# Performance work log

Hardware: AMD Instinct MI355X
Metric: run time of the kernel (lower is better)

Reference implementation:

```python
import jax, jax.numpy as jnp
import numpy as np

N_NODES = 100000
EPS = 1e-12  # F.normalize default eps


def _sage_conv(x, edge_index, Wl, bl, Wr):
    # PyG SAGEConv, aggr='mean', normalize=True.
    # edge_index[0] = source j, edge_index[1] = target i; messages flow j -> i.
    src, dst = edge_index[0], edge_index[1]
    msg_sum = jax.ops.segment_sum(x[src], dst, num_segments=N_NODES)  # [N, F]
    cnt = jax.ops.segment_sum(jnp.ones_like(src, dtype=x.dtype), dst,
                              num_segments=N_NODES)                  # [N]
    mean = msg_sum / jnp.maximum(cnt, 1.0)[:, None]  # empty neighborhoods -> 0
    out = mean @ Wl + bl + x @ Wr                    # lin_l(aggr) + lin_r(x)
    norm = jnp.sqrt(jnp.sum(out * out, axis=-1, keepdims=True))
    return out / jnp.maximum(norm, EPS)              # row-wise L2 normalize


def setup_inputs() -> dict:
    key = jax.random.key(0)
    ks = jax.random.split(key, 8)
    F_IN, F_HID, F_OUT = 64, 64, 32
    x = jax.random.normal(ks[0], (N_NODES, F_IN), dtype=jnp.float32)
    edge_index = jax.random.randint(ks[1], (2, 1000000), 0, N_NODES, dtype=jnp.int64)
    s1 = 1.0 / np.sqrt(F_IN)
    s2 = 1.0 / np.sqrt(F_HID)
    return {
        "x": x,
        "edge_index": edge_index,
        "W1l": jax.random.normal(ks[2], (F_IN, F_HID), dtype=jnp.float32) * s1,
        "b1": jnp.zeros((F_HID,), dtype=jnp.float32),
        "W1r": jax.random.normal(ks[3], (F_IN, F_HID), dtype=jnp.float32) * s1,
        "W2l": jax.random.normal(ks[4], (F_HID, F_OUT), dtype=jnp.float32) * s2,
        "b2": jnp.zeros((F_OUT,), dtype=jnp.float32),
        "W2r": jax.random.normal(ks[5], (F_HID, F_OUT), dtype=jnp.float32) * s2,
    }


def reference(x, edge_index, W1l, b1, W1r, W2l, b2, W2r):
    # eval mode: dropout(p=0.6) is identity
    h = jax.nn.relu(_sage_conv(x, edge_index, W1l, b1, W1r))
    out = _sage_conv(h, edge_index, W2l, b2, W2r)
    return out
```

## Files before the change

kernel.cpp:

```cpp
#include <hip/hip_runtime.h>

#define NN 100000
#define NE 1000000
#define NBK 391
#define CAP 3328
#define CH 8192
#define NCB ((NE + CH - 1) / CH)
#define PREP_ITEMS (NN * 16 + 64 + 64 * 128 + 32 * 128)
#define NPREPB ((PREP_ITEMS + 511) / 512)
#define XS 24.0f
#define HS 127.0f

typedef __attribute__((ext_vector_type(8))) short bf16x8;
typedef __attribute__((ext_vector_type(4))) float f32x4;

__device__ __forceinline__ ushort f2bf(float f) {
    uint u = __builtin_bit_cast(uint, f);
    u += 0x7FFFu + ((u >> 16) & 1u);
    return (ushort)(u >> 16);
}
__device__ __forceinline__ uint pack2(float a, float b) {
    uint ua = __builtin_bit_cast(uint, a), ub = __builtin_bit_cast(uint, b);
    ua += 0x7FFFu + ((ua >> 16) & 1u);
    ub += 0x7FFFu + ((ub >> 16) & 1u);
    return (ua >> 16) | (ub & 0xFFFF0000u);
}

__device__ __forceinline__ uint packi8(float4 v, float s) {
    int q0 = (int)rintf(fminf(fmaxf(v.x * s, -127.f), 127.f));
    int q1 = (int)rintf(fminf(fmaxf(v.y * s, -127.f), 127.f));
    int q2 = (int)rintf(fminf(fmaxf(v.z * s, -127.f), 127.f));
    int q3 = (int)rintf(fminf(fmaxf(v.w * s, -127.f), 127.f));
    return (q0 & 255) | ((q1 & 255) << 8) | ((q2 & 255) << 16) | ((q3 & 255) << 24);
}

#define DEC4(w, A0, A1, A2, A3)                                            \
    A0 += (float)((int)((w) << 24) >> 24);                                 \
    A1 += (float)((int)((w) << 16) >> 24);                                 \
    A2 += (float)((int)((w) << 8) >> 24);                                  \
    A3 += (float)((int)(w) >> 24);

#define ACCQ(p)                                                            \
    DEC4(p.x, a0, a1, a2, a3) DEC4(p.y, a4, a5, a6, a7)                    \
    DEC4(p.z, b0, b1, b2, b3) DEC4(p.w, b4, b5, b6, b7)


__global__ __launch_bounds__(512) void prep_bin(
    const float* __restrict__ x, uint* __restrict__ xb2, uint* __restrict__ x8w,
    const float* __restrict__ W1l, const float* __restrict__ W1r,
    const float* __restrict__ W2l, const float* __restrict__ W2r,
    ushort* __restrict__ W1t, ushort* __restrict__ W2t,
    uint* __restrict__ hb2, uint* __restrict__ h8w,
    const int* __restrict__ src, const int* __restrict__ dst,
    int* __restrict__ gcur, uint* __restrict__ binned) {
    int tid = threadIdx.x;
    if (blockIdx.x < NCB) {
        __shared__ int lh[NBK + 1], lb[NBK + 1], lr[NBK + 1];
        for (int i = tid; i < NBK + 1; i += 512) { lh[i] = 0; lr[i] = 0; }
        __syncthreads();
        int base = blockIdx.x * CH;
#pragma unroll
        for (int k = 0; k < 16; ++k) {
            int e = base + tid + k * 512;
            if (e < NE) atomicAdd(&lh[dst[e] >> 8], 1);
        }
        __syncthreads();
        if (tid < NBK && lh[tid] > 0)
            lb[tid] = tid * CAP + atomicAdd(&gcur[tid], lh[tid]);
        __syncthreads();
#pragma unroll
        for (int k = 0; k < 16; ++k) {
            int e = base + tid + k * 512;
            if (e < NE) {
                int d = dst[e];
                int bk = d >> 8;
                int r = atomicAdd(&lr[bk], 1);
                binned[lb[bk] + r] = (uint)src[e] | ((uint)(d & 255) << 24);
            }
        }
        return;
    }
    int t = (blockIdx.x - NCB) * 512 + tid;
    if (t < NN * 16) {
        float4 v = reinterpret_cast<const float4*>(x)[t];
        uint2 o;
        o.x = pack2(v.x, v.y);
        o.y = pack2(v.z, v.w);
        reinterpret_cast<uint2*>(xb2)[t] = o;
        int n = t >> 4, f0 = (t & 15) * 4;
        int pos = (f0 < 32) ? ((f0 >> 3) * 16 + (f0 & 7))
                            : (((f0 - 32) >> 3) * 16 + 8 + (f0 & 7));
        x8w[n * 16 + (pos >> 2)] = packi8(v, XS);
    } else {
        int z = t - NN * 16;
        if (z < 16) {
            uint2 o; o.x = 0u; o.y = 0u;
            reinterpret_cast<uint2*>(xb2)[NN * 16 + z] = o;
        } else if (z < 32) {
            uint2 o; o.x = 0u; o.y = 0u;
            reinterpret_cast<uint2*>(hb2)[NN * 16 + (z - 16)] = o;
        } else if (z < 48) {
            x8w[NN * 16 + (z - 32)] = 0u;
        } else if (z < 64) {
            h8w[NN * 16 + (z - 48)] = 0u;
        } else {
            int u = z - 64;
            if (u < 64 * 128) {
                int f = u >> 7, k = u & 127;
                float v = (k < 64) ? W1l[k * 64 + f] : W1r[(k - 64) * 64 + f];
                W1t[u] = f2bf(v);
            } else if (u < 64 * 128 + 32 * 128) {
                int p = u - 64 * 128;
                int f = p >> 7, k = p & 127;
                float v = (k < 64) ? W2l[k * 32 + f] : W2r[(k - 64) * 32 + f];
                W2t[p] = f2bf(v);
            }
        }
    }
}

__global__ __launch_bounds__(256) void sort_bucket(const uint* __restrict__ binned,
                                                   const int* __restrict__ gcur,
                                                   uint* __restrict__ ssrc,
                                                   uint* __restrict__ offp) {
    __shared__ uint recs[CAP];
    __shared__ int cnt[256], sc[256], cur[256];
    int b = blockIdx.x, t = threadIdx.x;
    int s = b * CAP, n = gcur[b];
    cnt[t] = 0;
    __syncthreads();
    for (int i = t; i < n; i += 256) {
        uint r = binned[s + i];
        recs[i] = r;
        atomicAdd(&cnt[r >> 24], 1);
    }
    __syncthreads();
    int c = cnt[t];
    int pc = (c + 3) & ~3;
    sc[t] = pc;
    for (int d = 1; d < 256; d <<= 1) {
        __syncthreads();
        int add = (t >= d) ? sc[t - d] : 0;
        __syncthreads();
        sc[t] += add;
    }
    __syncthreads();
    int ex = sc[t] - pc;
    cur[t] = ex;
    int node = b * 256 + t;
    if (node < NN) offp[node] = (uint)(s + ex) | ((uint)c << 22);
    __syncthreads();
    for (int i = t; i < n; i += 256) {
        uint r = recs[i];
        int p = atomicAdd(&cur[r >> 24], 1);
        ssrc[s + p] = r & 0xFFFFFFu;
    }
    for (int z = ex + c; z < ex + pc; ++z) ssrc[s + z] = NN;
}

__global__ __launch_bounds__(256) void layer1_fused(
    const uint4* __restrict__ x8v, const ushort* __restrict__ xb,
    const uint* __restrict__ offp, const uint* __restrict__ ssrc,
    const ushort* __restrict__ Wt, const float* __restrict__ bias,
    ushort* __restrict__ hb, uchar* __restrict__ h8) {
    int w = threadIdx.x >> 6, l = threadIdx.x & 63;
    int r = l & 15, q = l >> 4;
    int node0 = blockIdx.x * 64 + w * 16;
    int node = node0 + r;
    int beg = 0, c = 0;
    if (node < NN) {
        uint p = offp[node];
        beg = (int)(p & 0x3FFFFFu);
        c = (int)(p >> 22);
    }
    int rem = (c + 3) & ~3;
    float a0=0.f,a1=0.f,a2=0.f,a3=0.f,a4=0.f,a5=0.f,a6=0.f,a7=0.f;
    float b0=0.f,b1=0.f,b2=0.f,b3=0.f,b4=0.f,b5=0.f,b6=0.f,b7=0.f;
    int i = beg;
    uint j0 = 0, j1 = 0, j2 = 0, j3 = 0;
    if (rem > 0) { j0 = ssrc[i]; j1 = ssrc[i+1]; j2 = ssrc[i+2]; j3 = ssrc[i+3]; }
    while (rem > 0) {
        uint4 p0 = x8v[(size_t)j0 * 4 + q];
        uint4 p1 = x8v[(size_t)j1 * 4 + q];
        uint4 p2 = x8v[(size_t)j2 * 4 + q];
        uint4 p3 = x8v[(size_t)j3 * 4 + q];
        i += 4; rem -= 4;
        if (rem > 0) { j0 = ssrc[i]; j1 = ssrc[i+1]; j2 = ssrc[i+2]; j3 = ssrc[i+3]; }
        ACCQ(p0) ACCQ(p1) ACCQ(p2) ACCQ(p3)
    }
    float inv = 1.f / (fmaxf((float)c, 1.f) * XS);
    uint4 mu, mv;
    mu.x = pack2(a0 * inv, a1 * inv); mu.y = pack2(a2 * inv, a3 * inv);
    mu.z = pack2(a4 * inv, a5 * inv); mu.w = pack2(a6 * inv, a7 * inv);
    mv.x = pack2(b0 * inv, b1 * inv); mv.y = pack2(b2 * inv, b3 * inv);
    mv.z = pack2(b4 * inv, b5 * inv); mv.w = pack2(b6 * inv, b7 * inv);
    bf16x8 afr0 = __builtin_bit_cast(bf16x8, mu);
    bf16x8 afr1 = __builtin_bit_cast(bf16x8, mv);
    int arow = (node < NN) ? node : 0;
    const ushort* ax = xb + (size_t)arow * 64 + q * 8;
    bf16x8 afr2 = *reinterpret_cast<const bf16x8*>(ax);
    bf16x8 afr3 = *reinterpret_cast<const bf16x8*>(ax + 32);

    f32x4 c0 = {0.f, 0.f, 0.f, 0.f}, c1 = c0, c2 = c0, c3 = c0;
    const ushort* wp = Wt + (size_t)r * 128 + q * 8;
#pragma unroll
    for (int ks = 0; ks < 4; ++ks) {
        const ushort* wk = wp + ks * 32;
        bf16x8 w0 = *reinterpret_cast<const bf16x8*>(wk);
        bf16x8 w1 = *reinterpret_cast<const bf16x8*>(wk + 16 * 128);
        bf16x8 w2 = *reinterpret_cast<const bf16x8*>(wk + 32 * 128);
        bf16x8 w3 = *reinterpret_cast<const bf16x8*>(wk + 48 * 128);
        bf16x8 af = (ks == 0) ? afr0 : (ks == 1) ? afr1 : (ks == 2) ? afr2 : afr3;
        c0 = __builtin_amdgcn_mfma_f32_16x16x32_bf16(af, w0, c0, 0, 0, 0);
        c1 = __builtin_amdgcn_mfma_f32_16x16x32_bf16(af, w1, c1, 0, 0, 0);
        c2 = __builtin_amdgcn_mfma_f32_16x16x32_bf16(af, w2, c2, 0, 0, 0);
        c3 = __builtin_amdgcn_mfma_f32_16x16x32_bf16(af, w3, c3, 0, 0, 0);
    }
    float bb0 = bias[r], bb1 = bias[16 + r], bb2 = bias[32 + r], bb3 = bias[48 + r];
#pragma unroll
    for (int reg = 0; reg < 4; ++reg) {
        c0[reg] += bb0; c1[reg] += bb1; c2[reg] += bb2; c3[reg] += bb3;
    }
    int pr = (r >> 3) * 16, pj = r & 7;
#pragma unroll
    for (int reg = 0; reg < 4; ++reg) {
        float s = c0[reg] * c0[reg] + c1[reg] * c1[reg] +
                  c2[reg] * c2[reg] + c3[reg] * c3[reg];
        s += __shfl_xor(s, 1, 64);
        s += __shfl_xor(s, 2, 64);
        s += __shfl_xor(s, 4, 64);
        s += __shfl_xor(s, 8, 64);
        float scl = 1.f / fmaxf(sqrtf(s), 1e-12f);
        int grow = node0 + q * 4 + reg;
        if (grow < NN) {
            float v0 = fmaxf(c0[reg] * scl, 0.f);
            float v1 = fmaxf(c1[reg] * scl, 0.f);
            float v2 = fmaxf(c2[reg] * scl, 0.f);
            float v3 = fmaxf(c3[reg] * scl, 0.f);
            ushort* hp = hb + (size_t)grow * 64 + r;
            hp[0]  = f2bf(v0);
            hp[16] = f2bf(v1);
            hp[32] = f2bf(v2);
            hp[48] = f2bf(v3);
            uchar* hp8 = h8 + (size_t)grow * 64;
            hp8[pr + pj]           = (uchar)(int)rintf(v0 * HS);
            hp8[pr + 32 + pj]      = (uchar)(int)rintf(v1 * HS);
            hp8[pr + 8 + pj]       = (uchar)(int)rintf(v2 * HS);
            hp8[pr + 40 + pj]      = (uchar)(int)rintf(v3 * HS);
        }
    }
}

__global__ __launch_bounds__(256) void layer2_fused(
    const uint4* __restrict__ h8v, const ushort* __restrict__ hbuf,
    const uint* __restrict__ offp, const uint* __restrict__ ssrc,
    const ushort* __restrict__ Wt, const float* __restrict__ bias,
    float* __restrict__ out) {
    int w = threadIdx.x >> 6, l = threadIdx.x & 63;
    int r = l & 15, q = l >> 4;
    int node0 = blockIdx.x * 64 + w * 16;
    int node = node0 + r;
    int beg = 0, c = 0;
    if (node < NN) {
        uint p = offp[node];
        beg = (int)(p & 0x3FFFFFu);
        c = (int)(p >> 22);
    }
    int rem = (c + 3) & ~3;
    float a0=0.f,a1=0.f,a2=0.f,a3=0.f,a4=0.f,a5=0.f,a6=0.f,a7=0.f;
    float b0=0.f,b1=0.f,b2=0.f,b3=0.f,b4=0.f,b5=0.f,b6=0.f,b7=0.f;
    int i = beg;
    uint j0 = 0, j1 = 0, j2 = 0, j3 = 0;
    if (rem > 0) { j0 = ssrc[i]; j1 = ssrc[i+1]; j2 = ssrc[i+2]; j3 = ssrc[i+3]; }
    while (rem > 0) {
        uint4 p0 = h8v[(size_t)j0 * 4 + q];
        uint4 p1 = h8v[(size_t)j1 * 4 + q];
        uint4 p2 = h8v[(size_t)j2 * 4 + q];
        uint4 p3 = h8v[(size_t)j3 * 4 + q];
        i += 4; rem -= 4;
        if (rem > 0) { j0 = ssrc[i]; j1 = ssrc[i+1]; j2 = ssrc[i+2]; j3 = ssrc[i+3]; }
        ACCQ(p0) ACCQ(p1) ACCQ(p2) ACCQ(p3)
    }
    float inv = 1.f / (fmaxf((float)c, 1.f) * HS);
    uint4 mu, mv;
    mu.x = pack2(a0 * inv, a1 * inv); mu.y = pack2(a2 * inv, a3 * inv);
    mu.z = pack2(a4 * inv, a5 * inv); mu.w = pack2(a6 * inv, a7 * inv);
    mv.x = pack2(b0 * inv, b1 * inv); mv.y = pack2(b2 * inv, b3 * inv);
    mv.z = pack2(b4 * inv, b5 * inv); mv.w = pack2(b6 * inv, b7 * inv);
    bf16x8 afr0 = __builtin_bit_cast(bf16x8, mu);
    bf16x8 afr1 = __builtin_bit_cast(bf16x8, mv);
    int arow = (node < NN) ? node : 0;
    const ushort* ax = hbuf + (size_t)arow * 64 + q * 8;
    bf16x8 afr2 = *reinterpret_cast<const bf16x8*>(ax);
    bf16x8 afr3 = *reinterpret_cast<const bf16x8*>(ax + 32);

    f32x4 c0 = {0.f, 0.f, 0.f, 0.f}, c1 = c0;
    const ushort* wp = Wt + (size_t)r * 128 + q * 8;
#pragma unroll
    for (int ks = 0; ks < 4; ++ks) {
        const ushort* wk = wp + ks * 32;
        bf16x8 w0 = *reinterpret_cast<const bf16x8*>(wk);
        bf16x8 w1 = *reinterpret_cast<const bf16x8*>(wk + 16 * 128);
        bf16x8 af = (ks == 0) ? afr0 : (ks == 1) ? afr1 : (ks == 2) ? afr2 : afr3;
        c0 = __builtin_amdgcn_mfma_f32_16x16x32_bf16(af, w0, c0, 0, 0, 0);
        c1 = __builtin_amdgcn_mfma_f32_16x16x32_bf16(af, w1, c1, 0, 0, 0);
    }
    float bb0 = bias[r], bb1 = bias[16 + r];
#pragma unroll
    for (int reg = 0; reg < 4; ++reg) { c0[reg] += bb0; c1[reg] += bb1; }
#pragma unroll
    for (int reg = 0; reg < 4; ++reg) {
        float s = c0[reg] * c0[reg] + c1[reg] * c1[reg];
        s += __shfl_xor(s, 1, 64);
        s += __shfl_xor(s, 2, 64);
        s += __shfl_xor(s, 4, 64);
        s += __shfl_xor(s, 8, 64);
        float scl = 1.f / fmaxf(sqrtf(s), 1e-12f);
        int grow = node0 + q * 4 + reg;
        if (grow < NN) {
            float* op = out + (size_t)grow * 32 + r;
            op[0]  = c0[reg] * scl;
            op[16] = c1[reg] * scl;
        }
    }
}

extern "C" void kernel_launch(void* const* d_in, const int* in_sizes, int n_in,
                              void* d_out, int out_size, void* d_ws, size_t ws_size,
                              hipStream_t stream) {
    const float* x   = (const float*)d_in[0];
    const int*   ei  = (const int*)d_in[1];
    const int*   src = ei;
    const int*   dst = ei + NE;
    const float* W1l = (const float*)d_in[2];
    const float* b1  = (const float*)d_in[3];
    const float* W1r = (const float*)d_in[4];
    const float* W2l = (const float*)d_in[5];
    const float* b2  = (const float*)d_in[6];
    const float* W2r = (const float*)d_in[7];
    float* out = (float*)d_out;

    ushort* xb   = (ushort*)d_ws;
    ushort* hb   = xb + (size_t)(NN + 1) * 64;
    uchar*  x8   = (uchar*)(hb + (size_t)(NN + 1) * 64);
    uchar*  h8   = x8 + (size_t)(NN + 1) * 64;
    ushort* W1t  = (ushort*)(h8 + (size_t)(NN + 1) * 64);
    ushort* W2t  = W1t + 64 * 128;
    int*    gcur = (int*)(W2t + 32 * 128);
    uint*   offp = (uint*)(gcur + NBK + 1);
    uint*   binn = (uint*)(offp + NN);
    uint*   ssrc = binn + (size_t)NBK * CAP;

    hipMemsetAsync(gcur, 0, (NBK + 1) * sizeof(int), stream);

    prep_bin   <<<NCB + NPREPB, 512, 0, stream>>>(
                   x, (uint*)xb, (uint*)x8, W1l, W1r, W2l, W2r, W1t, W2t,
                   (uint*)hb, (uint*)h8, src, dst, gcur, binn);
    sort_bucket<<<NBK, 256, 0, stream>>>(binn, gcur, ssrc, offp);

    layer1_fused<<<(NN + 63) / 64, 256, 0, stream>>>(
                    (const uint4*)x8, xb, offp, ssrc, W1t, b1, hb, h8);
    layer2_fused<<<(NN + 63) / 64, 256, 0, stream>>>(
                    (const uint4*)h8, hb, offp, ssrc, W2t, b2, out);
}
```

Measured before the change: 97.21 us.

## Drop bf16 copy of x, use wave-shuffle scan, and widen gather unroll

The prep kernel no longer writes a bf16 copy of x. Layer 1 now reads the fp32 x rows directly and converts them to bf16 in registers, which removes a full-size write and read of that buffer. sort_bucket replaces the barrier-heavy shared-memory Hillis-Steele scan with a per-wave shuffle scan plus a combine across wave sums. Both gather loops now process 8 neighbors per iteration with the index loads issued inline rather than prefetched. In exchange, layer 1 reads twice as many bytes for its self term, and the prefetch of indices across iterations is gone.

After: 99.08 us. Within noise of the previous version (+1.9%).

```diff
diff --git a/kernel.cpp b/kernel.cpp
--- a/kernel.cpp
+++ b/kernel.cpp
@@ -6,7 +6,7 @@
 #define CAP 3328
 #define CH 8192
 #define NCB ((NE + CH - 1) / CH)
-#define PREP_ITEMS (NN * 16 + 64 + 64 * 128 + 32 * 128)
+#define PREP_ITEMS (NN * 16 + 32 + 64 * 128 + 32 * 128)
 #define NPREPB ((PREP_ITEMS + 511) / 512)
 #define XS 24.0f
 #define HS 127.0f
@@ -46,11 +46,11 @@
 
 
 __global__ __launch_bounds__(512) void prep_bin(
-    const float* __restrict__ x, uint* __restrict__ xb2, uint* __restrict__ x8w,
+    const float* __restrict__ x, uint* __restrict__ x8w,
     const float* __restrict__ W1l, const float* __restrict__ W1r,
     const float* __restrict__ W2l, const float* __restrict__ W2r,
     ushort* __restrict__ W1t, ushort* __restrict__ W2t,
-    uint* __restrict__ hb2, uint* __restrict__ h8w,
+    uint* __restrict__ h8w,
     const int* __restrict__ src, const int* __restrict__ dst,
     int* __restrict__ gcur, uint* __restrict__ binned) {
     int tid = threadIdx.x;
@@ -83,10 +83,6 @@
     int t = (blockIdx.x - NCB) * 512 + tid;
     if (t < NN * 16) {
         float4 v = reinterpret_cast<const float4*>(x)[t];
-        uint2 o;
-        o.x = pack2(v.x, v.y);
-        o.y = pack2(v.z, v.w);
-        reinterpret_cast<uint2*>(xb2)[t] = o;
         int n = t >> 4, f0 = (t & 15) * 4;
         int pos = (f0 < 32) ? ((f0 >> 3) * 16 + (f0 & 7))
                             : (((f0 - 32) >> 3) * 16 + 8 + (f0 & 7));
@@ -94,17 +90,11 @@
     } else {
         int z = t - NN * 16;
         if (z < 16) {
-            uint2 o; o.x = 0u; o.y = 0u;
-            reinterpret_cast<uint2*>(xb2)[NN * 16 + z] = o;
+            x8w[NN * 16 + z] = 0u;
         } else if (z < 32) {
-            uint2 o; o.x = 0u; o.y = 0u;
-            reinterpret_cast<uint2*>(hb2)[NN * 16 + (z - 16)] = o;
-        } else if (z < 48) {
-            x8w[NN * 16 + (z - 32)] = 0u;
-        } else if (z < 64) {
-            h8w[NN * 16 + (z - 48)] = 0u;
+            h8w[NN * 16 + (z - 16)] = 0u;
         } else {
-            int u = z - 64;
+            int u = z - 32;
             if (u < 64 * 128) {
                 int f = u >> 7, k = u & 127;
                 float v = (k < 64) ? W1l[k * 64 + f] : W1r[(k - 64) * 64 + f];
@@ -124,7 +114,7 @@
                                                    uint* __restrict__ ssrc,
                                                    uint* __restrict__ offp) {
     __shared__ uint recs[CAP];
-    __shared__ int cnt[256], sc[256], cur[256];
+    __shared__ int cnt[256], cur[256], wsum[4];
     int b = blockIdx.x, t = threadIdx.x;
     int s = b * CAP, n = gcur[b];
     cnt[t] = 0;
@@ -137,15 +127,19 @@
     __syncthreads();
     int c = cnt[t];
     int pc = (c + 3) & ~3;
-    sc[t] = pc;
-    for (int d = 1; d < 256; d <<= 1) {
-        __syncthreads();
-        int add = (t >= d) ? sc[t - d] : 0;
-        __syncthreads();
-        sc[t] += add;
-    }
+    int lane = t & 63, wid = t >> 6;
+    int v = pc;
+#pragma unroll
+    for (int d = 1; d < 64; d <<= 1) {
+        int o = __shfl_up(v, d, 64);
+        if (lane >= d) v += o;
+    }
+    if (lane == 63) wsum[wid] = v;
     __syncthreads();
-    int ex = sc[t] - pc;
+    int wpre = 0;
+#pragma unroll
+    for (int ww = 0; ww < 3; ++ww) wpre += (ww < wid) ? wsum[ww] : 0;
+    int ex = wpre + v - pc;
     cur[t] = ex;
     int node = b * 256 + t;
     if (node < NN) offp[node] = (uint)(s + ex) | ((uint)c << 22);
@@ -159,7 +153,7 @@
 }
 
 __global__ __launch_bounds__(256) void layer1_fused(
-    const uint4* __restrict__ x8v, const ushort* __restrict__ xb,
+    const uint4* __restrict__ x8v, const float* __restrict__ x,
     const uint* __restrict__ offp, const uint* __restrict__ ssrc,
     const ushort* __restrict__ Wt, const float* __restrict__ bias,
     ushort* __restrict__ hb, uchar* __restrict__ h8) {
@@ -177,15 +171,26 @@
     float a0=0.f,a1=0.f,a2=0.f,a3=0.f,a4=0.f,a5=0.f,a6=0.f,a7=0.f;
     float b0=0.f,b1=0.f,b2=0.f,b3=0.f,b4=0.f,b5=0.f,b6=0.f,b7=0.f;
     int i = beg;
-    uint j0 = 0, j1 = 0, j2 = 0, j3 = 0;
-    if (rem > 0) { j0 = ssrc[i]; j1 = ssrc[i+1]; j2 = ssrc[i+2]; j3 = ssrc[i+3]; }
-    while (rem > 0) {
+    while (rem >= 8) {
+        uint j0 = ssrc[i],     j1 = ssrc[i + 1], j2 = ssrc[i + 2], j3 = ssrc[i + 3];
+        uint j4 = ssrc[i + 4], j5 = ssrc[i + 5], j6 = ssrc[i + 6], j7 = ssrc[i + 7];
         uint4 p0 = x8v[(size_t)j0 * 4 + q];
         uint4 p1 = x8v[(size_t)j1 * 4 + q];
         uint4 p2 = x8v[(size_t)j2 * 4 + q];
         uint4 p3 = x8v[(size_t)j3 * 4 + q];
-        i += 4; rem -= 4;
-        if (rem > 0) { j0 = ssrc[i]; j1 = ssrc[i+1]; j2 = ssrc[i+2]; j3 = ssrc[i+3]; }
+        uint4 p4 = x8v[(size_t)j4 * 4 + q];
+        uint4 p5 = x8v[(size_t)j5 * 4 + q];
+        uint4 p6 = x8v[(size_t)j6 * 4 + q];
+        uint4 p7 = x8v[(size_t)j7 * 4 + q];
+        i += 8; rem -= 8;
+        ACCQ(p0) ACCQ(p1) ACCQ(p2) ACCQ(p3) ACCQ(p4) ACCQ(p5) ACCQ(p6) ACCQ(p7)
+    }
+    if (rem > 0) {
+        uint j0 = ssrc[i], j1 = ssrc[i + 1], j2 = ssrc[i + 2], j3 = ssrc[i + 3];
+        uint4 p0 = x8v[(size_t)j0 * 4 + q];
+        uint4 p1 = x8v[(size_t)j1 * 4 + q];
+        uint4 p2 = x8v[(size_t)j2 * 4 + q];
+        uint4 p3 = x8v[(size_t)j3 * 4 + q];
         ACCQ(p0) ACCQ(p1) ACCQ(p2) ACCQ(p3)
     }
     float inv = 1.f / (fmaxf((float)c, 1.f) * XS);
@@ -197,9 +202,16 @@
     bf16x8 afr0 = __builtin_bit_cast(bf16x8, mu);
     bf16x8 afr1 = __builtin_bit_cast(bf16x8, mv);
     int arow = (node < NN) ? node : 0;
-    const ushort* ax = xb + (size_t)arow * 64 + q * 8;
-    bf16x8 afr2 = *reinterpret_cast<const bf16x8*>(ax);
-    bf16x8 afr3 = *reinterpret_cast<const bf16x8*>(ax + 32);
+    const float4* xf = reinterpret_cast<const float4*>(x) + (size_t)arow * 16 + q * 2;
+    float4 s0 = xf[0], s1 = xf[1];
+    float4 s2 = xf[8], s3 = xf[9];
+    uint4 su, sv;
+    su.x = pack2(s0.x, s0.y); su.y = pack2(s0.z, s0.w);
+    su.z = pack2(s1.x, s1.y); su.w = pack2(s1.z, s1.w);
+    sv.x = pack2(s2.x, s2.y); sv.y = pack2(s2.z, s2.w);
+    sv.z = pack2(s3.x, s3.y); sv.w = pack2(s3.z, s3.w);
+    bf16x8 afr2 = __builtin_bit_cast(bf16x8, su);
+    bf16x8 afr3 = __builtin_bit_cast(bf16x8, sv);
 
     f32x4 c0 = {0.f, 0.f, 0.f, 0.f}, c1 = c0, c2 = c0, c3 = c0;
     const ushort* wp = Wt + (size_t)r * 128 + q * 8;
@@ -243,10 +255,10 @@
             hp[32] = f2bf(v2);
             hp[48] = f2bf(v3);
             uchar* hp8 = h8 + (size_t)grow * 64;
-            hp8[pr + pj]           = (uchar)(int)rintf(v0 * HS);
-            hp8[pr + 32 + pj]      = (uchar)(int)rintf(v1 * HS);
-            hp8[pr + 8 + pj]       = (uchar)(int)rintf(v2 * HS);
-            hp8[pr + 40 + pj]      = (uchar)(int)rintf(v3 * HS);
+            hp8[pr + pj]      = (uchar)(int)rintf(v0 * HS);
+            hp8[pr + 32 + pj] = (uchar)(int)rintf(v1 * HS);
+            hp8[pr + 8 + pj]  = (uchar)(int)rintf(v2 * HS);
+            hp8[pr + 40 + pj] = (uchar)(int)rintf(v3 * HS);
         }
     }
 }
@@ -270,15 +282,26 @@
     float a0=0.f,a1=0.f,a2=0.f,a3=0.f,a4=0.f,a5=0.f,a6=0.f,a7=0.f;
     float b0=0.f,b1=0.f,b2=0.f,b3=0.f,b4=0.f,b5=0.f,b6=0.f,b7=0.f;
     int i = beg;
-    uint j0 = 0, j1 = 0, j2 = 0, j3 = 0;
-    if (rem > 0) { j0 = ssrc[i]; j1 = ssrc[i+1]; j2 = ssrc[i+2]; j3 = ssrc[i+3]; }
-    while (rem > 0) {
+    while (rem >= 8) {
+        uint j0 = ssrc[i],     j1 = ssrc[i + 1], j2 = ssrc[i + 2], j3 = ssrc[i + 3];
+        uint j4 = ssrc[i + 4], j5 = ssrc[i + 5], j6 = ssrc[i + 6], j7 = ssrc[i + 7];
         uint4 p0 = h8v[(size_t)j0 * 4 + q];
         uint4 p1 = h8v[(size_t)j1 * 4 + q];
         uint4 p2 = h8v[(size_t)j2 * 4 + q];
         uint4 p3 = h8v[(size_t)j3 * 4 + q];
-        i += 4; rem -= 4;
-        if (rem > 0) { j0 = ssrc[i]; j1 = ssrc[i+1]; j2 = ssrc[i+2]; j3 = ssrc[i+3]; }
+        uint4 p4 = h8v[(size_t)j4 * 4 + q];
+        uint4 p5 = h8v[(size_t)j5 * 4 + q];
+        uint4 p6 = h8v[(size_t)j6 * 4 + q];
+        uint4 p7 = h8v[(size_t)j7 * 4 + q];
+        i += 8; rem -= 8;
+        ACCQ(p0) ACCQ(p1) ACCQ(p2) ACCQ(p3) ACCQ(p4) ACCQ(p5) ACCQ(p6) ACCQ(p7)
+    }
+    if (rem > 0) {
+        uint j0 = ssrc[i], j1 = ssrc[i + 1], j2 = ssrc[i + 2], j3 = ssrc[i + 3];
+        uint4 p0 = h8v[(size_t)j0 * 4 + q];
+        uint4 p1 = h8v[(size_t)j1 * 4 + q];
+        uint4 p2 = h8v[(size_t)j2 * 4 + q];
+        uint4 p3 = h8v[(size_t)j3 * 4 + q];
         ACCQ(p0) ACCQ(p1) ACCQ(p2) ACCQ(p3)
     }
     float inv = 1.f / (fmaxf((float)c, 1.f) * HS);
@@ -340,9 +363,8 @@
     const float* W2r = (const float*)d_in[7];
     float* out = (float*)d_out;
 
-    ushort* xb   = (ushort*)d_ws;
-    ushort* hb   = xb + (size_t)(NN + 1) * 64;
-    uchar*  x8   = (uchar*)(hb + (size_t)(NN + 1) * 64);
+    ushort* hb   = (ushort*)d_ws;
+    uchar*  x8   = (uchar*)(hb + (size_t)NN * 64);
     uchar*  h8   = x8 + (size_t)(NN + 1) * 64;
     ushort* W1t  = (ushort*)(h8 + (size_t)(NN + 1) * 64);
     ushort* W2t  = W1t + 64 * 128;
@@ -354,12 +376,12 @@
     hipMemsetAsync(gcur, 0, (NBK + 1) * sizeof(int), stream);
 
     prep_bin   <<<NCB + NPREPB, 512, 0, stream>>>(
-                   x, (uint*)xb, (uint*)x8, W1l, W1r, W2l, W2r, W1t, W2t,
-                   (uint*)hb, (uint*)h8, src, dst, gcur, binn);
+                   x, (uint*)x8, W1l, W1r, W2l, W2r, W1t, W2t,
+                   (uint*)h8, src, dst, gcur, binn);
     sort_bucket<<<NBK, 256, 0, stream>>>(binn, gcur, ssrc, offp);
 
     layer1_fused<<<(NN + 63) / 64, 256, 0, stream>>>(
-                    (const uint4*)x8, xb, offp, ssrc, W1t, b1, hb, h8);
+                    (const uint4*)x8, x, offp, ssrc, W1t, b1, hb, h8);
     layer2_fused<<<(NN + 63) / 64, 256, 0, stream>>>(
                     (const uint4*)h8, hb, offp, ssrc, W2t, b2, out);
 }
```
